# Optimization experiments

Hardware: AMD Instinct MI355X
Metric: run time of the kernel (lower is better)

Reference implementation:

```python
import jax, jax.numpy as jnp
import numpy as np

H = 256      # HIDDEN_DIM
F_IN = 16    # input_dim
B = 512
S = 168      # encoder sequence length
T = 24       # PRED_LEN


def _lstm_cell(x, h, c, w_ih, w_hh, b):
    # torch gate order: i, f, g, o
    g = x @ w_ih.T + h @ w_hh.T + b
    i, f, gg, o = jnp.split(g, 4, axis=-1)
    c_new = jax.nn.sigmoid(f) * c + jax.nn.sigmoid(i) * jnp.tanh(gg)
    h_new = jax.nn.sigmoid(o) * jnp.tanh(c_new)
    return h_new, c_new


def _lstm_layer(x, w_ih, w_hh, b):
    # x: [S, B, in] -> outputs [S, B, H], final (h, c)
    Bv, Hv = x.shape[1], w_hh.shape[1]
    init = (jnp.zeros((Bv, Hv), x.dtype), jnp.zeros((Bv, Hv), x.dtype))
    def step(carry, xt):
        h, c = _lstm_cell(xt, carry[0], carry[1], w_ih, w_hh, b)
        return (h, c), h
    (h, c), ys = jax.lax.scan(step, init, x)
    return ys, h, c


def setup_inputs() -> dict:
    key = jax.random.key(0)
    ks = jax.random.split(key, 24)
    s = 1.0 / np.sqrt(H)
    u = lambda k, shape: jax.random.uniform(k, shape, jnp.float32, -s, s)
    inp = {}
    inp['src'] = jax.random.normal(ks[0], (B, S, F_IN), jnp.float32)
    # encoder LSTM (2 layers); biases b_ih + b_hh fused into one vector
    inp['enc_w_ih0'] = u(ks[1], (4 * H, F_IN))
    inp['enc_w_hh0'] = u(ks[2], (4 * H, H))
    inp['enc_b0'] = u(ks[3], (4 * H,))
    inp['enc_w_ih1'] = u(ks[4], (4 * H, H))
    inp['enc_w_hh1'] = u(ks[5], (4 * H, H))
    inp['enc_b1'] = u(ks[6], (4 * H,))
    # decoder LSTM (2 layers), input_size = 1 + H
    inp['dec_w_ih0'] = u(ks[7], (4 * H, 1 + H))
    inp['dec_w_hh0'] = u(ks[8], (4 * H, H))
    inp['dec_b0'] = u(ks[9], (4 * H,))
    inp['dec_w_ih1'] = u(ks[10], (4 * H, H))
    inp['dec_w_hh1'] = u(ks[11], (4 * H, H))
    inp['dec_b1'] = u(ks[12], (4 * H,))
    # attention: Linear(2H -> H), v: Linear(H -> 1, no bias), position bias
    inp['attn_w'] = u(ks[13], (H, 2 * H))
    inp['attn_b'] = u(ks[14], (H,))
    inp['attn_v'] = u(ks[15], (H,))
    inp['pos_bias'] = jax.random.normal(ks[16], (H,), jnp.float32)
    # fc_out: Linear(H -> 1)
    inp['fc_w'] = u(ks[17], (1, H))
    inp['fc_b'] = u(ks[18], (1,))
    return inp


def reference(src, enc_w_ih0, enc_w_hh0, enc_b0, enc_w_ih1, enc_w_hh1, enc_b1,
              dec_w_ih0, dec_w_hh0, dec_b0, dec_w_ih1, dec_w_hh1, dec_b1,
              attn_w, attn_b, attn_v, pos_bias, fc_w, fc_b):
    x = jnp.transpose(src, (1, 0, 2))  # [S, B, F]
    y0, _, _ = _lstm_layer(x, enc_w_ih0, enc_w_hh0, enc_b0)
    enc_out_t, h1e, c1e = _lstm_layer(y0, enc_w_ih1, enc_w_hh1, enc_b1)
    # also need final state of layer 0 for decoder init
    h0e, c0e = y0[-1], None
    # recompute layer-0 final cell state: rerun scan carry output
    # (cheap alternative: _lstm_layer returns (ys, h, c); reuse it)
    _, h0e, c0e = _lstm_layer(x, enc_w_ih0, enc_w_hh0, enc_b0)
    enc_out = jnp.transpose(enc_out_t, (1, 0, 2))  # [B, S, H]

    We, Wd = attn_w[:, :H], attn_w[:, H:]
    enc_proj = jnp.einsum('bsh,gh->bsg', enc_out, We)  # precomputed encoder projection
    dec_in0 = src[:, -1, -1:]  # [B, 1]

    def dec_step(carry, t):
        h0, c0, h1, c1, dec_in = carry
        # additive attention using top-layer decoder hidden
        e = jnp.tanh(enc_proj + (h1 @ Wd.T + attn_b)[:, None, :])
        e = e + pos_bias[None, None, :] * (t / 24.0)
        w = jax.nn.softmax(e @ attn_v, axis=1)              # [B, S]
        ctx = jnp.einsum('bs,bsh->bh', w, enc_out)          # [B, H]
        x0 = jnp.concatenate([dec_in, ctx], axis=1)          # [B, 1+H]
        h0n, c0n = _lstm_cell(x0, h0, c0, dec_w_ih0, dec_w_hh0, dec_b0)
        h1n, c1n = _lstm_cell(h0n, h1, c1, dec_w_ih1, dec_w_hh1, dec_b1)
        pred = h1n @ fc_w.T + fc_b                           # [B, 1]
        # NOTE: the gated blend of decoder_output in the source is dead code
        # (the blended tensor is never used), so it is omitted here.
        return (h0n, c0n, h1n, c1n, pred), pred

    ts = jnp.arange(T, dtype=src.dtype)
    _, preds = jax.lax.scan(dec_step, (h0e, c0e, h1e, c1e, dec_in0), ts)
    return jnp.transpose(preds, (1, 0, 2))  # [B, T, 1]
```

## Files before the change

### kernel.cpp

```cpp
#include <hip/hip_runtime.h>
#include <hip/hip_fp16.h>
#include <math.h>

#define BB 512
#define HH 256
#define SS 168
#define TT 24
#define NBLK 256
#define NTHR 256
typedef unsigned long long ull;
typedef unsigned short u16;
#define BH 131072ull

#define O_Y0  0ull
#define O_H1  262144ull
#define O_H0  524288ull
#define O_CTX 786432ull
#define O_W0  933888ull
#define O_W1  1261568ull
#define O_WP  2834432ull
#define O_WDT 2835456ull
#define O_BP  2900992ull
#define O_E16 2905088ull
#define O_P16 13915136ull

typedef float f32x4 __attribute__((ext_vector_type(4)));
typedef float v2f __attribute__((ext_vector_type(2)));
typedef unsigned int ru4 __attribute__((ext_vector_type(4)));

__device__ __forceinline__ float sigf(float x) { return 1.f / (1.f + expf(-x)); }

#define AR __ATOMIC_RELAXED
#define SCA __HIP_MEMORY_SCOPE_AGENT
__device__ __forceinline__ int aLd(int* p) { return __hip_atomic_load(p, AR, SCA); }
__device__ __forceinline__ int aAdd(int* p, int v) { return __hip_atomic_fetch_add(p, v, AR, SCA); }

__device__ __forceinline__ float2 ld2(const float* p) {
  ull raw = __hip_atomic_load((const ull*)p, AR, SCA);
  float2 v; v.x = __uint_as_float((unsigned)raw); v.y = __uint_as_float((unsigned)(raw >> 32));
  return v;
}
__device__ __forceinline__ float ld1(const float* p) {
  unsigned raw = __hip_atomic_load((const unsigned*)p, AR, SCA);
  return __uint_as_float(raw);
}
__device__ __forceinline__ void st1(float* p, float v) {
  __hip_atomic_store((unsigned*)p, __float_as_uint(v), AR, SCA);
}
__device__ __forceinline__ void sth(__half* p, __half v) {
  __hip_atomic_store((unsigned short*)p, __half_as_ushort(v), AR, SCA);
}
__device__ __forceinline__ void stu(unsigned* p, unsigned v) {
  __hip_atomic_store(p, v, AR, SCA);
}

__device__ __forceinline__ void ld_h(const float* p, v2f& a, v2f& b) {
  asm volatile("global_load_dwordx2 %0, %2, off sc0 sc1\n\t"
               "global_load_dwordx2 %1, %3, off sc0 sc1"
               : "=&v"(a), "=&v"(b) : "v"(p), "v"(p + 16) : "memory");
}
struct W4 { ru4 v[4]; };
__device__ __forceinline__ void ld_w4(const u16* ph, const u16* pl, W4& w) {
  asm volatile("global_load_dwordx4 %0, %4, off\n\t"
               "global_load_dwordx4 %1, %5, off\n\t"
               "global_load_dwordx4 %2, %6, off\n\t"
               "global_load_dwordx4 %3, %7, off"
               : "=&v"(w.v[0]), "=&v"(w.v[1]), "=&v"(w.v[2]), "=&v"(w.v[3])
               : "v"(ph), "v"(ph + 8), "v"(pl), "v"(pl + 8) : "memory");
}
#define VMW(n) asm volatile("s_waitcnt vmcnt(" #n ")" ::: "memory")

#define MFMA(d, a, b) asm volatile("v_mfma_f32_16x16x32_bf16 %0, %1, %2, %0" \
                                   : "+v"(d) : "v"(a), "v"(b))
#define TOUCH(x) asm volatile("" : "+v"(x))

__device__ __forceinline__ void poll(int* f, int tgt) {
  while (aLd(f) < tgt) __builtin_amdgcn_s_sleep(1);
}
__device__ __forceinline__ void flag_arrive(int* f) {
  asm volatile("s_waitcnt vmcnt(0)" ::: "memory");
  __syncthreads();
  if (threadIdx.x == 0) aAdd(f, 1);
}
__device__ __forceinline__ void flag_wait2(int* f0, int t0, int* f1, int t1) {
  if (threadIdx.x == 0 && f0) poll(f0, t0);
  if (threadIdx.x == 64 && f1) poll(f1, t1);
  __syncthreads();
}

struct SMT {
  union {
    struct { unsigned WsH[128][20]; unsigned WsL[128][20]; float Ht[32][36]; } m;
    struct { float As[32][65];  float Bs[32][65]; } g;
    struct { float h1s[256], qs[256], vs[256], sc[192], ctxs[512], sred[4]; } at;
  };
};

__device__ __forceinline__ void fma16(float acc[4][4], const float4 hv, const float4 wv) {
  acc[0][0] += hv.x * wv.x; acc[0][1] += hv.x * wv.y; acc[0][2] += hv.x * wv.z; acc[0][3] += hv.x * wv.w;
  acc[1][0] += hv.y * wv.x; acc[1][1] += hv.y * wv.y; acc[1][2] += hv.y * wv.z; acc[1][3] += hv.y * wv.w;
  acc[2][0] += hv.z * wv.x; acc[2][1] += hv.z * wv.y; acc[2][2] += hv.z * wv.z; acc[2][3] += hv.z * wv.w;
  acc[3][0] += hv.w * wv.x; acc[3][1] += hv.w * wv.y; acc[3][2] += hv.w * wv.z; acc[3][3] += hv.w * wv.w;
}

__device__ __forceinline__ unsigned rne16(unsigned u) {
  return (u + 0x7fffu + ((u >> 16) & 1u)) >> 16;
}
__device__ __forceinline__ void split8v(const f32x4 a, const f32x4 b, ru4& hi, ru4& lo) {
#pragma unroll
  for (int j = 0; j < 4; j++) {
    const float x = (j < 2) ? a[2 * j] : b[2 * j - 4];
    const float y = (j < 2) ? a[2 * j + 1] : b[2 * j - 3];
    const unsigned hx = rne16(__float_as_uint(x)), hy = rne16(__float_as_uint(y));
    const float rx = x - __uint_as_float(hx << 16);
    const float ry = y - __uint_as_float(hy << 16);
    hi[j] = (hx & 0xffffu) | (hy << 16);
    lo[j] = (rne16(__float_as_uint(rx)) & 0xffffu) | (rne16(__float_as_uint(ry)) << 16);
  }
}

__device__ __forceinline__ void comp_mfma(SMT& sm, int wq, int w1, int l15, int l4,
                                          f32x4 acc[4])
{
  const int hr = w1 * 16 + l15;
  const f32x4 hv0 = *(const f32x4*)&sm.m.Ht[hr][l4 * 8];
  const f32x4 hv1 = *(const f32x4*)&sm.m.Ht[hr][l4 * 8 + 4];
  ru4 bhi, blo;
  split8v(hv0, hv1, bhi, blo);
  asm volatile("s_nop 1" : "+v"(bhi), "+v"(blo));
#pragma unroll
  for (int g = 0; g < 4; g++) {
    const int cr = wq * 64 + g * 16 + l15;
    ru4 ah = *(const ru4*)&sm.m.WsH[cr][l4 * 4];
    ru4 al = *(const ru4*)&sm.m.WsL[cr][l4 * 4];
    MFMA(acc[g], ah, bhi);
    MFMA(acc[g], ah, blo);
    MFMA(acc[g], al, bhi);
  }
}

#define STW(wv) do { \
  *(ru4*)&sm.m.WsH[cgt][kt * 8]     = (wv).v[0]; \
  *(ru4*)&sm.m.WsH[cgt][kt * 8 + 4] = (wv).v[1]; \
  *(ru4*)&sm.m.WsL[cgt][kt * 8]     = (wv).v[2]; \
  *(ru4*)&sm.m.WsL[cgt][kt * 8 + 4] = (wv).v[3]; } while (0)
#define STH(a, b) do { \
  sm.m.Ht[r][p2 * 2]      = (a)[0]; sm.m.Ht[r][p2 * 2 + 1]  = (a)[1]; \
  sm.m.Ht[r][p2 * 2 + 16] = (b)[0]; sm.m.Ht[r][p2 * 2 + 17] = (b)[1]; } while (0)

__device__ void gemm_pipe(const u16* wbh, const u16* wbl,
                          const float* hb0, const float* hb1,
                          int NC, int nc0, f32x4 acc[4], SMT& sm,
                          int wq, int w1, int l15, int l4)
{
  const int tid = threadIdx.x;
  const int r = tid & 31, p2 = tid >> 5;
  const int cgt = tid & 127, kt = tid >> 7;
  const float* h1p = hb1 - (ull)nc0 * 32;
#define HBk(k) (((k) < nc0) ? (hb0 + (k) * 32) : (h1p + (k) * 32))
  W4 wr0, wr1, wr2, wr3;
  v2f h0a, h0b, h1a, h1b, h2a, h2b, h3a, h3b;
  ld_w4(wbh, wbl, wr0);
  ld_h(HBk(0), h0a, h0b);
  ld_w4(wbh + 32, wbl + 32, wr1);
  ld_h(HBk(1), h1a, h1b);
  ld_h(HBk(2), h2a, h2b);
  for (int c = 0; c < NC; c += 4) {
    VMW(8);
    STW(wr0); STH(h0a, h0b);
    __syncthreads();
    ld_w4(wbh + (c + 2) * 32, wbl + (c + 2) * 32, wr2);
    ld_h(HBk(c + 3), h3a, h3b);
    comp_mfma(sm, wq, w1, l15, l4, acc);
    __syncthreads();
    VMW(8);
    STW(wr1); STH(h1a, h1b);
    __syncthreads();
    ld_w4(wbh + (c + 3) * 32, wbl + (c + 3) * 32, wr3);
    ld_h(HBk(c + 4), h0a, h0b);
    comp_mfma(sm, wq, w1, l15, l4, acc);
    __syncthreads();
    VMW(8);
    STW(wr2); STH(h2a, h2b);
    __syncthreads();
    ld_w4(wbh + (c + 4) * 32, wbl + (c + 4) * 32, wr0);
    ld_h(HBk(c + 5), h1a, h1b);
    comp_mfma(sm, wq, w1, l15, l4, acc);
    __syncthreads();
    VMW(8);
    STW(wr3); STH(h3a, h3b);
    __syncthreads();
    ld_w4(wbh + (c + 5) * 32, wbl + (c + 5) * 32, wr1);
    ld_h(HBk(c + 6), h2a, h2b);
    comp_mfma(sm, wq, w1, l15, l4, acc);
    __syncthreads();
  }
  asm volatile("s_waitcnt vmcnt(0)" ::: "memory");
  asm volatile("s_nop 7\n\ts_nop 7"
               : "+v"(acc[0]), "+v"(acc[1]), "+v"(acc[2]), "+v"(acc[3]));
#undef HBk
}

__device__ __forceinline__ void lstm_epi4(f32x4 acc[4], float cR[4], int row, int ubase, int l4,
                                          float* hout, __half* e16, int sstep)
{
#pragma unroll
  for (int g = 0; g < 4; g++) {
    const int u = ubase + g * 4 + l4;
    const float iv = sigf(acc[g][0]), fv = sigf(acc[g][1]);
    const float gv = tanhf(acc[g][2]), ov = sigf(acc[g][3]);
    const float cn = fv * cR[g] + iv * gv;
    cR[g] = cn;
    const float hn = ov * tanhf(cn);
    st1(hout + (ull)row * 256 + u, hn);
    if (e16) sth(e16 + ((ull)row * SS + sstep) * 256 + u, __float2half(hn));
  }
}

__device__ void attn_fc(int row, int t, int slot, const float* h1r, const float* wdT,
                        const float* attn_b, const float* attn_v,
                        const __half* P16, const __half* E16,
                        const float* fc_w, const float* fc_b,
                        float* ctxb, float* out, SMT& sm)
{
  const int tid = threadIdx.x;
  __syncthreads();
  if (tid < 128) {
    float2 v = ld2(h1r + (ull)slot * BH + (ull)row * 256 + tid * 2);
    sm.at.h1s[tid * 2] = v.x; sm.at.h1s[tid * 2 + 1] = v.y;
  }
  __syncthreads();
  if (t >= 1 && tid < 64) {
    float a = 0.f;
#pragma unroll
    for (int j = 0; j < 4; j++) a += sm.at.h1s[tid + 64 * j] * fc_w[tid + 64 * j];
#pragma unroll
    for (int m = 32; m >= 1; m >>= 1) a += __shfl_xor(a, m, 64);
    if (tid == 0) {
      const float p = a + fc_b[0];
      out[(ull)row * TT + (t - 1)] = p;
      st1(ctxb + (ull)row * 288 + 256, p);
    }
  }
  if (t >= TT) return;
  float qv = attn_b[tid];
  for (int k = 0; k < 256; k += 4) {
    qv += sm.at.h1s[k]     * wdT[(ull)(k)     * 256 + tid];
    qv += sm.at.h1s[k + 1] * wdT[(ull)(k + 1) * 256 + tid];
    qv += sm.at.h1s[k + 2] * wdT[(ull)(k + 2) * 256 + tid];
    qv += sm.at.h1s[k + 3] * wdT[(ull)(k + 3) * 256 + tid];
  }
  sm.at.qs[tid] = qv;
  sm.at.vs[tid] = attn_v[tid];
  __syncthreads();
  const int wv = tid >> 6, lane = tid & 63;
  for (int s = wv; s < SS; s += 4) {
    const __half2* Pr = (const __half2*)(P16 + ((ull)row * SS + s) * 256);
    float a = 0.f;
#pragma unroll
    for (int jj = 0; jj < 2; jj++) {
      const int i2 = lane + 64 * jj;
      const float2 pv = __half22float2(Pr[i2]);
      const int g0 = i2 * 2;
      a += sm.at.vs[g0] * tanhf(pv.x + sm.at.qs[g0]);
      a += sm.at.vs[g0 + 1] * tanhf(pv.y + sm.at.qs[g0 + 1]);
    }
#pragma unroll
    for (int m = 32; m >= 1; m >>= 1) a += __shfl_xor(a, m, 64);
    if (lane == 0) sm.at.sc[s] = a;
  }
  __syncthreads();
  if (tid < 64) {
    float m = -1e30f;
    for (int i = tid; i < SS; i += 64) m = fmaxf(m, sm.at.sc[i]);
#pragma unroll
    for (int mm = 32; mm >= 1; mm >>= 1) m = fmaxf(m, __shfl_xor(m, mm, 64));
    if (tid == 0) sm.at.sred[0] = m;
  }
  __syncthreads();
  const float smax = sm.at.sred[0];
  if (tid < SS) sm.at.sc[tid] = expf(sm.at.sc[tid] - smax);
  __syncthreads();
  if (tid < 64) {
    float ssum = 0.f;
    for (int i = tid; i < SS; i += 64) ssum += sm.at.sc[i];
#pragma unroll
    for (int mm = 32; mm >= 1; mm >>= 1) ssum += __shfl_xor(ssum, mm, 64);
    if (tid == 0) sm.at.sred[1] = ssum;
  }
  __syncthreads();
  const float rinv = 1.f / sm.at.sred[1];
  const int u2 = tid & 127, sh = tid >> 7;
  float cx = 0.f, cy = 0.f;
  for (int s = sh * 84; s < sh * 84 + 84; s++) {
    const float w = sm.at.sc[s] * rinv;
    const float2 ev = __half22float2(*(const __half2*)(E16 + ((ull)row * SS + s) * 256 + u2 * 2));
    cx += w * ev.x; cy += w * ev.y;
  }
  sm.at.ctxs[sh * 256 + u2 * 2] = cx;
  sm.at.ctxs[sh * 256 + u2 * 2 + 1] = cy;
  __syncthreads();
  st1(ctxb + (ull)row * 288 + tid, sm.at.ctxs[tid] + sm.at.ctxs[256 + tid]);
}

__device__ void proj_tile(const __half* E16, const float* attn_w, __half* P16,
                          int m0, int n0, SMT& sm)
{
  const int tid = threadIdx.x;
  const int mq = tid & 15, nq = tid >> 4;
  const int li = tid & 63, kq = tid >> 6;
  float acc[4][4] = {{0.f}};
  for (int k0 = 0; k0 < 256; k0 += 32) {
    float4 raw = *(const float4*)(E16 + (ull)(m0 + li) * 256 + k0 + kq * 8);
    const __half* hp = (const __half*)&raw;
#pragma unroll
    for (int i = 0; i < 8; i++) sm.g.As[kq * 8 + i][li] = __half2float(hp[i]);
    const float* gb = attn_w + (ull)(n0 + li) * 512 + k0 + kq * 8;
    const float4 v0 = *(const float4*)gb, v1 = *(const float4*)(gb + 4);
    sm.g.Bs[kq * 8 + 0][li] = v0.x; sm.g.Bs[kq * 8 + 1][li] = v0.y;
    sm.g.Bs[kq * 8 + 2][li] = v0.z; sm.g.Bs[kq * 8 + 3][li] = v0.w;
    sm.g.Bs[kq * 8 + 4][li] = v1.x; sm.g.Bs[kq * 8 + 5][li] = v1.y;
    sm.g.Bs[kq * 8 + 6][li] = v1.z; sm.g.Bs[kq * 8 + 7][li] = v1.w;
    __syncthreads();
#pragma unroll 8
    for (int kk = 0; kk < 32; kk++) {
      const float4 a4 = *(const float4*)&sm.g.As[kk][mq * 4];
      const float4 b4 = *(const float4*)&sm.g.Bs[kk][nq * 4];
      fma16(acc, a4, b4);
    }
    __syncthreads();
  }
#pragma unroll
  for (int i = 0; i < 4; i++) {
    const int m = m0 + mq * 4 + i;
#pragma unroll
    for (int j = 0; j < 2; j++) {
      __half2 h2; h2.x = __float2half(acc[i][j * 2]); h2.y = __float2half(acc[i][j * 2 + 1]);
      stu((unsigned*)(P16 + (ull)m * 256 + n0 + nq * 4) + j, *(unsigned*)&h2);
    }
  }
}

__global__ __launch_bounds__(256, 1) void seq2seq_pipe(
    const float* __restrict__ src,
    const float* __restrict__ attn_w, const float* __restrict__ attn_b,
    const float* __restrict__ attn_v,
    const float* __restrict__ fc_w, const float* __restrict__ fc_b,
    float* __restrict__ out, int* __restrict__ ib)
{
  __shared__ SMT sm;
  const int blk = blockIdx.x;
  const int tid = threadIdx.x;
  float* fb = (float*)ib + 65536;
  float* y0r  = fb + O_Y0;
  float* h1r  = fb + O_H1;
  float* h0r  = fb + O_H0;
  float* zb   = h0r + BH;
  float* ctxb = fb + O_CTX;
  const u16* whi0 = (const u16*)(fb + O_W0);
  const u16* wlo0 = whi0 + 1024ull * 320;
  const u16* whi1 = (const u16*)(fb + O_W1);
  const u16* wlo1 = whi1 + 1024ull * 512;
  const u16* dhi0 = whi1 + 2ull * 1024 * 512;
  const u16* dlo0 = whi1 + 3ull * 1024 * 512;
  const u16* dhi1 = whi1 + 4ull * 1024 * 512;
  const u16* dlo1 = whi1 + 5ull * 1024 * 512;
  const float* wp  = fb + O_WP;
  const float* wdT = fb + O_WDT;
  const float* bp  = fb + O_BP;
  __half* E16 = (__half*)(fb + O_E16);
  __half* P16 = (__half*)(fb + O_P16);
  const int g = blk >> 5, m = blk & 31;
  const int rowg = g * 64;
  int* gf = ib + g * 1024;
  int* ife = gf;
  int* ifa = gf + 704; int* ifh0 = gf + 736; int* ifh1 = gf + 768; int* ifp = gf + 900;

  const int lm = (m < 16) ? m : (m - 16);
  const int row0 = rowg + (lm & 1) * 32;
  const int gc0 = (lm >> 1) * 128;
  const int w = tid >> 6;
  const int l15 = tid & 15, l4 = (tid >> 4) & 3;
  const int wq = w >> 1, w1 = w & 1;
  const int gcw = gc0 + wq * 64;
  const int myrow = row0 + w1 * 16 + l15;
  const int ubase = gcw >> 2;
  const int r = tid & 31;
  const int cgt = tid & 127, kt = tid >> 7;

  float cReg[4] = {0.f, 0.f, 0.f, 0.f};

  for (int t = 0; t <= SS; t++) {
    flag_wait2(t ? ife + (t - 1) : nullptr, 32, nullptr, 0);
    if (m < 16) {
      if (t < SS) {
        f32x4 acc[4];
#pragma unroll
        for (int gg = 0; gg < 4; gg++) {
          acc[gg] = *(const f32x4*)(bp + gcw + gg * 16 + l4 * 4);
          TOUCH(acc[gg]);
        }
        {
          W4 wx;
          ld_w4(whi0 + (ull)(gc0 + cgt) * 320 + kt * 16,
                wlo0 + (ull)(gc0 + cgt) * 320 + kt * 16, wx);
          VMW(0);
          *(ru4*)&sm.m.WsH[cgt][kt * 8]     = wx.v[0];
          *(ru4*)&sm.m.WsH[cgt][kt * 8 + 4] = wx.v[1];
          *(ru4*)&sm.m.WsL[cgt][kt * 8]     = wx.v[2];
          *(ru4*)&sm.m.WsL[cgt][kt * 8 + 4] = wx.v[3];
          const int f = tid >> 5;
          sm.m.Ht[r][f]      = src[((ull)(row0 + r) * SS + t) * 16 + f];
          sm.m.Ht[r][f + 8]  = src[((ull)(row0 + r) * SS + t) * 16 + f + 8];
          sm.m.Ht[r][f + 16] = 0.f;
          sm.m.Ht[r][f + 24] = 0.f;
          __syncthreads();
          comp_mfma(sm, wq, w1, l15, l4, acc);
          __syncthreads();
        }
        const float* ysrc = (t == 0) ? zb : (y0r + (ull)((t + 1) & 1) * BH);
        const float* hb0 = ysrc + (ull)(row0 + r) * 256 + (tid >> 5) * 2;
        gemm_pipe(whi0 + (ull)(gc0 + cgt) * 320 + 32 + kt * 16,
                  wlo0 + (ull)(gc0 + cgt) * 320 + 32 + kt * 16,
                  hb0, hb0, 8, 8, acc, sm, wq, w1, l15, l4);
        lstm_epi4(acc, cReg, myrow, ubase, l4, y0r + (ull)(t & 1) * BH, nullptr, 0);
      }
    } else {
      if (t >= 1) {
        const int s = t - 1;
        f32x4 acc[4];
#pragma unroll
        for (int gg = 0; gg < 4; gg++) {
          acc[gg] = *(const f32x4*)(bp + 1024 + gcw + gg * 16 + l4 * 4);
          TOUCH(acc[gg]);
        }
        const float* ysrc = y0r + (ull)(s & 1) * BH;
        const float* hsrc = (s == 0) ? zb : (h1r + (ull)((s + 1) & 1) * BH);
        const float* hb0 = ysrc + (ull)(row0 + r) * 256 + (tid >> 5) * 2;
        const float* hb1 = hsrc + (ull)(row0 + r) * 256 + (tid >> 5) * 2;
        gemm_pipe(whi1 + (ull)(gc0 + cgt) * 512 + kt * 16,
                  wlo1 + (ull)(gc0 + cgt) * 512 + kt * 16,
                  hb0, hb1, 16, 8, acc, sm, wq, w1, l15, l4);
        lstm_epi4(acc, cReg, myrow, ubase, l4, h1r + (ull)(s & 1) * BH, E16, s);
      }
    }
    flag_arrive(ife + t);
  }

  if (tid == 0) poll(ife + SS, 32);
  __syncthreads();
  {
    const int em0 = rowg * SS;
    for (int tau = m; tau < 672; tau += 32)
      proj_tile(E16, attn_w, P16, em0 + (tau >> 2) * 64, (tau & 3) * 64, sm);
  }
  flag_arrive(ifp);

  for (int t = 0; t <= TT; t++) {
    if (t == 0) flag_wait2(ifp, 32, nullptr, 0);
    else flag_wait2(ifh1 + (t - 1), 16, nullptr, 0);
    const int slot = (t + 1) & 1;
    attn_fc(rowg + 2 * m,     t, slot, h1r, wdT, attn_b, attn_v, P16, E16, fc_w, fc_b, ctxb, out, sm);
    attn_fc(rowg + 2 * m + 1, t, slot, h1r, wdT, attn_b, attn_v, P16, E16, fc_w, fc_b, ctxb, out, sm);
    if (t == TT) break;
    flag_arrive(ifa + t);
    if (m < 16) {
      flag_wait2(ifa + t, 32, t ? ifh0 + (t - 1) : nullptr, 16);
      f32x4 acc[4];
#pragma unroll
      for (int gg = 0; gg < 4; gg++) {
        acc[gg] = *(const f32x4*)(bp + 2048 + gcw + gg * 16 + l4 * 4);
        TOUCH(acc[gg]);
      }
      const float* h0src = (t == 0) ? (y0r + BH) : (h0r + (ull)((t + 1) & 1) * BH);
      const float* hb0 = ctxb + (ull)(row0 + r) * 288 + (tid >> 5) * 2;
      const float* hb1 = h0src + (ull)(row0 + r) * 256 + (tid >> 5) * 2;
      gemm_pipe(dhi0 + (ull)(gc0 + cgt) * 512 + kt * 16,
                dlo0 + (ull)(gc0 + cgt) * 512 + kt * 16,
                hb0, hb1, 16, 8, acc, sm, wq, w1, l15, l4);
      const float p = ld1(ctxb + (ull)myrow * 288 + 256);
#pragma unroll
      for (int gg = 0; gg < 4; gg++) {
        const f32x4 wpv = *(const f32x4*)(wp + gcw + gg * 16 + l4 * 4);
        acc[gg] = acc[gg] + wpv * p;
      }
      lstm_epi4(acc, cReg, myrow, ubase, l4, h0r + (ull)(t & 1) * BH, nullptr, 0);
      flag_arrive(ifh0 + t);
    } else {
      flag_wait2(ifh0 + t, 16, t ? ifh1 + (t - 1) : nullptr, 16);
      f32x4 acc[4];
#pragma unroll
      for (int gg = 0; gg < 4; gg++) {
        acc[gg] = *(const f32x4*)(bp + 3072 + gcw + gg * 16 + l4 * 4);
        TOUCH(acc[gg]);
      }
      const float* hb0 = h0r + (ull)(t & 1) * BH + (ull)(row0 + r) * 256 + (tid >> 5) * 2;
      const float* hb1 = h1r + (ull)((t + 1) & 1) * BH + (ull)(row0 + r) * 256 + (tid >> 5) * 2;
      gemm_pipe(dhi1 + (ull)(gc0 + cgt) * 512 + kt * 16,
                dlo1 + (ull)(gc0 + cgt) * 512 + kt * 16,
                hb0, hb1, 16, 8, acc, sm, wq, w1, l15, l4);
      lstm_epi4(acc, cReg, myrow, ubase, l4, h1r + (ull)(t & 1) * BH, nullptr, 0);
      flag_arrive(ifh1 + t);
    }
  }
}

__device__ __forceinline__ void split_store(float v, u16* hi, u16* lo, ull i) {
  const unsigned u = __float_as_uint(v);
  const unsigned hb = (u + 0x7fffu + ((u >> 16) & 1u)) >> 16;
  const float rr = v - __uint_as_float(hb << 16);
  const unsigned ur = __float_as_uint(rr);
  const unsigned lb = (ur + 0x7fffu + ((ur >> 16) & 1u)) >> 16;
  hi[i] = (u16)hb; lo[i] = (u16)lb;
}

__global__ void init_all(
    const float* __restrict__ src,
    const float* __restrict__ ewih0, const float* __restrict__ ewhh0, const float* __restrict__ eb0,
    const float* __restrict__ ewih1, const float* __restrict__ ewhh1, const float* __restrict__ eb1,
    const float* __restrict__ dwih0, const float* __restrict__ dwhh0, const float* __restrict__ db0,
    const float* __restrict__ dwih1, const float* __restrict__ dwhh1, const float* __restrict__ db1,
    const float* __restrict__ attn_w, int* __restrict__ ib)
{
  const int gid = blockIdx.x * 256 + threadIdx.x;
  const int NG = 1024 * 256;
  float* fb = (float*)ib + 65536;
  u16* whi0 = (u16*)(fb + O_W0);
  u16* wlo0 = whi0 + 1024ull * 320;
  u16* whi1 = (u16*)(fb + O_W1);
  u16* wlo1 = whi1 + 1024ull * 512;
  u16* dhi0 = whi1 + 2ull * 1024 * 512;
  u16* dlo0 = whi1 + 3ull * 1024 * 512;
  u16* dhi1 = whi1 + 4ull * 1024 * 512;
  u16* dlo1 = whi1 + 5ull * 1024 * 512;
  float* wpd = fb + O_WP;

  for (int i = gid; i < 8192; i += NG) ib[i] = 0;
  for (int i = gid; i < (int)BH; i += NG) fb[O_H0 + BH + i] = 0.f;
  for (int i = gid; i < 1024 * 320; i += NG) {
    const int cg = i / 320, k = i - cg * 320, j = (cg & 3) * 256 + (cg >> 2);
    float v = 0.f;
    if (k < 16) v = ewih0[(ull)j * 16 + k];
    else if (k >= 32 && k < 288) v = ewhh0[(ull)j * 256 + (k - 32)];
    split_store(v, whi0, wlo0, i);
  }
  for (int i = gid; i < 1024 * 512; i += NG) {
    const int cg = i >> 9, k = i & 511, j = (cg & 3) * 256 + (cg >> 2);
    split_store((k < 256) ? ewih1[(ull)j * 256 + k] : ewhh1[(ull)j * 256 + k - 256], whi1, wlo1, i);
    split_store((k < 256) ? dwih0[(ull)j * 257 + 1 + k] : dwhh0[(ull)j * 256 + k - 256], dhi0, dlo0, i);
    split_store((k < 256) ? dwih1[(ull)j * 256 + k] : dwhh1[(ull)j * 256 + k - 256], dhi1, dlo1, i);
  }
  for (int i = gid; i < 1024; i += NG) {
    const int j = (i & 3) * 256 + (i >> 2);
    wpd[i] = dwih0[(ull)j * 257];
  }
  for (int i = gid; i < 256 * 256; i += NG) {
    const int k = i >> 8, gg = i & 255;
    fb[O_WDT + i] = attn_w[(ull)gg * 512 + 256 + k];
  }
  for (int i = gid; i < 4096; i += NG) {
    const int set = i >> 10, cg = i & 1023, j = (cg & 3) * 256 + (cg >> 2);
    const float* bsrc = (set == 0) ? eb0 : (set == 1) ? eb1 : (set == 2) ? db0 : db1;
    fb[O_BP + i] = bsrc[j];
  }
  for (int i = gid; i < 512; i += NG)
    fb[O_CTX + (ull)i * 288 + 256] = src[((ull)i * SS + 167) * 16 + 15];
}

extern "C" void kernel_launch(void* const* d_in, const int* in_sizes, int n_in,
                              void* d_out, int out_size, void* d_ws, size_t ws_size,
                              hipStream_t stream)
{
  const float* src    = (const float*)d_in[0];
  const float* ewih0  = (const float*)d_in[1];
  const float* ewhh0  = (const float*)d_in[2];
  const float* eb0    = (const float*)d_in[3];
  const float* ewih1  = (const float*)d_in[4];
  const float* ewhh1  = (const float*)d_in[5];
  const float* eb1    = (const float*)d_in[6];
  const float* dwih0  = (const float*)d_in[7];
  const float* dwhh0  = (const float*)d_in[8];
  const float* db0    = (const float*)d_in[9];
  const float* dwih1  = (const float*)d_in[10];
  const float* dwhh1  = (const float*)d_in[11];
  const float* db1    = (const float*)d_in[12];
  const float* attn_w = (const float*)d_in[13];
  const float* attn_b = (const float*)d_in[14];
  const float* attn_v = (const float*)d_in[15];
  const float* fc_w   = (const float*)d_in[17];
  const float* fc_b   = (const float*)d_in[18];
  float* out = (float*)d_out;
  int* ib    = (int*)d_ws;

  init_all<<<1024, 256, 0, stream>>>(src, ewih0, ewhh0, eb0, ewih1, ewhh1, eb1,
                                     dwih0, dwhh0, db0, dwih1, dwhh1, db1, attn_w, ib);

  void* args[] = {
    (void*)&src, (void*)&attn_w, (void*)&attn_b, (void*)&attn_v,
    (void*)&fc_w, (void*)&fc_b, (void*)&out, (void*)&ib,
  };
  hipError_t lerr = hipLaunchCooperativeKernel((const void*)seq2seq_pipe, dim3(NBLK), dim3(NTHR),
                                               args, 0, stream);
  if (lerr != hipSuccess) {
    hipLaunchKernelGGL(seq2seq_pipe, dim3(NBLK), dim3(NTHR), 0, stream,
                       src, attn_w, attn_b, attn_v, fc_w, fc_b, out, ib);
  }
}
```

Before: 7.867 ms.

## Double threads per block to 512 and split per-thread GEMM and attention work

Raises the persistent kernel's block size from 256 to 512 threads. Each warp now covers 32 gate columns instead of 64 in the MFMA LSTM GEMM, and per-thread weight and hidden loads are halved. The attention score and context loops are spread over 8 waves, with four partial context sums reduced at the end. The intent is more latency hiding and shorter per-thread serial chains in the latency-bound recurrent steps, at the cost of more registers per block, idle threads in the projection tile, and heavier barriers.

```diff
diff --git a/kernel.cpp b/kernel.cpp
--- a/kernel.cpp
+++ b/kernel.cpp
@@ -7,7 +7,7 @@
 #define SS 168
 #define TT 24
 #define NBLK 256
-#define NTHR 256
+#define NTHR 512
 typedef unsigned long long ull;
 typedef unsigned short u16;
 #define BH 131072ull
@@ -54,19 +54,14 @@
   __hip_atomic_store(p, v, AR, SCA);
 }
 
-__device__ __forceinline__ void ld_h(const float* p, v2f& a, v2f& b) {
-  asm volatile("global_load_dwordx2 %0, %2, off sc0 sc1\n\t"
-               "global_load_dwordx2 %1, %3, off sc0 sc1"
-               : "=&v"(a), "=&v"(b) : "v"(p), "v"(p + 16) : "memory");
-}
-struct W4 { ru4 v[4]; };
-__device__ __forceinline__ void ld_w4(const u16* ph, const u16* pl, W4& w) {
-  asm volatile("global_load_dwordx4 %0, %4, off\n\t"
-               "global_load_dwordx4 %1, %5, off\n\t"
-               "global_load_dwordx4 %2, %6, off\n\t"
-               "global_load_dwordx4 %3, %7, off"
-               : "=&v"(w.v[0]), "=&v"(w.v[1]), "=&v"(w.v[2]), "=&v"(w.v[3])
-               : "v"(ph), "v"(ph + 8), "v"(pl), "v"(pl + 8) : "memory");
+__device__ __forceinline__ void ld_h2(const float* p, v2f& a) {
+  asm volatile("global_load_dwordx2 %0, %1, off sc0 sc1"
+               : "=&v"(a) : "v"(p) : "memory");
+}
+__device__ __forceinline__ void ld_w2(const u16* ph, const u16* pl, ru4& h, ru4& l) {
+  asm volatile("global_load_dwordx4 %0, %2, off\n\t"
+               "global_load_dwordx4 %1, %3, off"
+               : "=&v"(h), "=&v"(l) : "v"(ph), "v"(pl) : "memory");
 }
 #define VMW(n) asm volatile("s_waitcnt vmcnt(" #n ")" ::: "memory")
 
@@ -92,7 +87,7 @@
   union {
     struct { unsigned WsH[128][20]; unsigned WsL[128][20]; float Ht[32][36]; } m;
     struct { float As[32][65];  float Bs[32][65]; } g;
-    struct { float h1s[256], qs[256], vs[256], sc[192], ctxs[512], sred[4]; } at;
+    struct { float h1s[256], qs[256], vs[256], sc[192], ctxs[1024], sred[4]; } at;
   };
 };
 
@@ -120,7 +115,7 @@
 }
 
 __device__ __forceinline__ void comp_mfma(SMT& sm, int wq, int w1, int l15, int l4,
-                                          f32x4 acc[4])
+                                          f32x4 acc[2])
 {
   const int hr = w1 * 16 + l15;
   const f32x4 hv0 = *(const f32x4*)&sm.m.Ht[hr][l4 * 8];
@@ -129,8 +124,8 @@
   split8v(hv0, hv1, bhi, blo);
   asm volatile("s_nop 1" : "+v"(bhi), "+v"(blo));
 #pragma unroll
-  for (int g = 0; g < 4; g++) {
-    const int cr = wq * 64 + g * 16 + l15;
+  for (int g = 0; g < 2; g++) {
+    const int cr = wq * 32 + g * 16 + l15;
     ru4 ah = *(const ru4*)&sm.m.WsH[cr][l4 * 4];
     ru4 al = *(const ru4*)&sm.m.WsL[cr][l4 * 4];
     MFMA(acc[g], ah, bhi);
@@ -139,18 +134,15 @@
   }
 }
 
-#define STW(wv) do { \
-  *(ru4*)&sm.m.WsH[cgt][kt * 8]     = (wv).v[0]; \
-  *(ru4*)&sm.m.WsH[cgt][kt * 8 + 4] = (wv).v[1]; \
-  *(ru4*)&sm.m.WsL[cgt][kt * 8]     = (wv).v[2]; \
-  *(ru4*)&sm.m.WsL[cgt][kt * 8 + 4] = (wv).v[3]; } while (0)
-#define STH(a, b) do { \
-  sm.m.Ht[r][p2 * 2]      = (a)[0]; sm.m.Ht[r][p2 * 2 + 1]  = (a)[1]; \
-  sm.m.Ht[r][p2 * 2 + 16] = (b)[0]; sm.m.Ht[r][p2 * 2 + 17] = (b)[1]; } while (0)
+#define STW(wh, wl) do { \
+  *(ru4*)&sm.m.WsH[cgt][kt * 4] = (wh); \
+  *(ru4*)&sm.m.WsL[cgt][kt * 4] = (wl); } while (0)
+#define STH(a) do { \
+  sm.m.Ht[r][p2 * 2] = (a)[0]; sm.m.Ht[r][p2 * 2 + 1] = (a)[1]; } while (0)
 
 __device__ void gemm_pipe(const u16* wbh, const u16* wbl,
                           const float* hb0, const float* hb1,
-                          int NC, int nc0, f32x4 acc[4], SMT& sm,
+                          int NC, int nc0, f32x4 acc[2], SMT& sm,
                           int wq, int w1, int l15, int l4)
 {
   const int tid = threadIdx.x;
@@ -158,54 +150,53 @@
   const int cgt = tid & 127, kt = tid >> 7;
   const float* h1p = hb1 - (ull)nc0 * 32;
 #define HBk(k) (((k) < nc0) ? (hb0 + (k) * 32) : (h1p + (k) * 32))
-  W4 wr0, wr1, wr2, wr3;
-  v2f h0a, h0b, h1a, h1b, h2a, h2b, h3a, h3b;
-  ld_w4(wbh, wbl, wr0);
-  ld_h(HBk(0), h0a, h0b);
-  ld_w4(wbh + 32, wbl + 32, wr1);
-  ld_h(HBk(1), h1a, h1b);
-  ld_h(HBk(2), h2a, h2b);
+  ru4 wh0, wl0, wh1, wl1, wh2, wl2, wh3, wl3;
+  v2f h0, h1, h2, h3;
+  ld_w2(wbh,      wbl,      wh0, wl0);
+  ld_h2(HBk(0), h0);
+  ld_w2(wbh + 32, wbl + 32, wh1, wl1);
+  ld_h2(HBk(1), h1);
+  ld_h2(HBk(2), h2);
   for (int c = 0; c < NC; c += 4) {
-    VMW(8);
-    STW(wr0); STH(h0a, h0b);
-    __syncthreads();
-    ld_w4(wbh + (c + 2) * 32, wbl + (c + 2) * 32, wr2);
-    ld_h(HBk(c + 3), h3a, h3b);
+    VMW(4);
+    STW(wh0, wl0); STH(h0);
+    __syncthreads();
+    ld_w2(wbh + (c + 2) * 32, wbl + (c + 2) * 32, wh2, wl2);
+    ld_h2(HBk(c + 3), h3);
     comp_mfma(sm, wq, w1, l15, l4, acc);
     __syncthreads();
-    VMW(8);
-    STW(wr1); STH(h1a, h1b);
-    __syncthreads();
-    ld_w4(wbh + (c + 3) * 32, wbl + (c + 3) * 32, wr3);
-    ld_h(HBk(c + 4), h0a, h0b);
+    VMW(4);
+    STW(wh1, wl1); STH(h1);
+    __syncthreads();
+    ld_w2(wbh + (c + 3) * 32, wbl + (c + 3) * 32, wh3, wl3);
+    ld_h2(HBk(c + 4), h0);
     comp_mfma(sm, wq, w1, l15, l4, acc);
     __syncthreads();
-    VMW(8);
-    STW(wr2); STH(h2a, h2b);
-    __syncthreads();
-    ld_w4(wbh + (c + 4) * 32, wbl + (c + 4) * 32, wr0);
-    ld_h(HBk(c + 5), h1a, h1b);
+    VMW(4);
+    STW(wh2, wl2); STH(h2);
+    __syncthreads();
+    ld_w2(wbh + (c + 4) * 32, wbl + (c + 4) * 32, wh0, wl0);
+    ld_h2(HBk(c + 5), h1);
     comp_mfma(sm, wq, w1, l15, l4, acc);
     __syncthreads();
-    VMW(8);
-    STW(wr3); STH(h3a, h3b);
-    __syncthreads();
-    ld_w4(wbh + (c + 5) * 32, wbl + (c + 5) * 32, wr1);
-    ld_h(HBk(c + 6), h2a, h2b);
+    VMW(4);
+    STW(wh3, wl3); STH(h3);
+    __syncthreads();
+    ld_w2(wbh + (c + 5) * 32, wbl + (c + 5) * 32, wh1, wl1);
+    ld_h2(HBk(c + 6), h2);
     comp_mfma(sm, wq, w1, l15, l4, acc);
     __syncthreads();
   }
   asm volatile("s_waitcnt vmcnt(0)" ::: "memory");
-  asm volatile("s_nop 7\n\ts_nop 7"
-               : "+v"(acc[0]), "+v"(acc[1]), "+v"(acc[2]), "+v"(acc[3]));
+  asm volatile("s_nop 7\n\ts_nop 7" : "+v"(acc[0]), "+v"(acc[1]));
 #undef HBk
 }
 
-__device__ __forceinline__ void lstm_epi4(f32x4 acc[4], float cR[4], int row, int ubase, int l4,
+__device__ __forceinline__ void lstm_epi2(f32x4 acc[2], float cR[2], int row, int ubase, int l4,
                                           float* hout, __half* e16, int sstep)
 {
 #pragma unroll
-  for (int g = 0; g < 4; g++) {
+  for (int g = 0; g < 2; g++) {
     const int u = ubase + g * 4 + l4;
     const float iv = sigf(acc[g][0]), fv = sigf(acc[g][1]);
     const float gv = tanhf(acc[g][2]), ov = sigf(acc[g][3]);
@@ -243,18 +234,20 @@
     }
   }
   if (t >= TT) return;
-  float qv = attn_b[tid];
-  for (int k = 0; k < 256; k += 4) {
-    qv += sm.at.h1s[k]     * wdT[(ull)(k)     * 256 + tid];
-    qv += sm.at.h1s[k + 1] * wdT[(ull)(k + 1) * 256 + tid];
-    qv += sm.at.h1s[k + 2] * wdT[(ull)(k + 2) * 256 + tid];
-    qv += sm.at.h1s[k + 3] * wdT[(ull)(k + 3) * 256 + tid];
-  }
-  sm.at.qs[tid] = qv;
-  sm.at.vs[tid] = attn_v[tid];
+  if (tid < 256) {
+    float qv = attn_b[tid];
+    for (int k = 0; k < 256; k += 4) {
+      qv += sm.at.h1s[k]     * wdT[(ull)(k)     * 256 + tid];
+      qv += sm.at.h1s[k + 1] * wdT[(ull)(k + 1) * 256 + tid];
+      qv += sm.at.h1s[k + 2] * wdT[(ull)(k + 2) * 256 + tid];
+      qv += sm.at.h1s[k + 3] * wdT[(ull)(k + 3) * 256 + tid];
+    }
+    sm.at.qs[tid] = qv;
+    sm.at.vs[tid] = attn_v[tid];
+  }
   __syncthreads();
   const int wv = tid >> 6, lane = tid & 63;
-  for (int s = wv; s < SS; s += 4) {
+  for (int s = wv; s < SS; s += 8) {
     const __half2* Pr = (const __half2*)(P16 + ((ull)row * SS + s) * 256);
     float a = 0.f;
 #pragma unroll
@@ -292,7 +285,7 @@
   const float rinv = 1.f / sm.at.sred[1];
   const int u2 = tid & 127, sh = tid >> 7;
   float cx = 0.f, cy = 0.f;
-  for (int s = sh * 84; s < sh * 84 + 84; s++) {
+  for (int s = sh * 42; s < sh * 42 + 42; s++) {
     const float w = sm.at.sc[s] * rinv;
     const float2 ev = __half22float2(*(const __half2*)(E16 + ((ull)row * SS + s) * 256 + u2 * 2));
     cx += w * ev.x; cy += w * ev.y;
@@ -300,48 +293,57 @@
   sm.at.ctxs[sh * 256 + u2 * 2] = cx;
   sm.at.ctxs[sh * 256 + u2 * 2 + 1] = cy;
   __syncthreads();
-  st1(ctxb + (ull)row * 288 + tid, sm.at.ctxs[tid] + sm.at.ctxs[256 + tid]);
+  if (tid < 256)
+    st1(ctxb + (ull)row * 288 + tid,
+        sm.at.ctxs[tid] + sm.at.ctxs[256 + tid] + sm.at.ctxs[512 + tid] + sm.at.ctxs[768 + tid]);
 }
 
 __device__ void proj_tile(const __half* E16, const float* attn_w, __half* P16,
                           int m0, int n0, SMT& sm)
 {
   const int tid = threadIdx.x;
-  const int mq = tid & 15, nq = tid >> 4;
-  const int li = tid & 63, kq = tid >> 6;
+  const bool act = tid < 256;
+  const int mq = tid & 15, nq = (tid >> 4) & 15;
+  const int li = tid & 63, kq = (tid >> 6) & 3;
   float acc[4][4] = {{0.f}};
   for (int k0 = 0; k0 < 256; k0 += 32) {
-    float4 raw = *(const float4*)(E16 + (ull)(m0 + li) * 256 + k0 + kq * 8);
-    const __half* hp = (const __half*)&raw;
-#pragma unroll
-    for (int i = 0; i < 8; i++) sm.g.As[kq * 8 + i][li] = __half2float(hp[i]);
-    const float* gb = attn_w + (ull)(n0 + li) * 512 + k0 + kq * 8;
-    const float4 v0 = *(const float4*)gb, v1 = *(const float4*)(gb + 4);
-    sm.g.Bs[kq * 8 + 0][li] = v0.x; sm.g.Bs[kq * 8 + 1][li] = v0.y;
-    sm.g.Bs[kq * 8 + 2][li] = v0.z; sm.g.Bs[kq * 8 + 3][li] = v0.w;
-    sm.g.Bs[kq * 8 + 4][li] = v1.x; sm.g.Bs[kq * 8 + 5][li] = v1.y;
-    sm.g.Bs[kq * 8 + 6][li] = v1.z; sm.g.Bs[kq * 8 + 7][li] = v1.w;
-    __syncthreads();
+    if (act) {
+      float4 raw = *(const float4*)(E16 + (ull)(m0 + li) * 256 + k0 + kq * 8);
+      const __half* hp = (const __half*)&raw;
+#pragma unroll
+      for (int i = 0; i < 8; i++) sm.g.As[kq * 8 + i][li] = __half2float(hp[i]);
+      const float* gb = attn_w + (ull)(n0 + li) * 512 + k0 + kq * 8;
+      const float4 v0 = *(const float4*)gb, v1 = *(const float4*)(gb + 4);
+      sm.g.Bs[kq * 8 + 0][li] = v0.x; sm.g.Bs[kq * 8 + 1][li] = v0.y;
+      sm.g.Bs[kq * 8 + 2][li] = v0.z; sm.g.Bs[kq * 8 + 3][li] = v0.w;
+      sm.g.Bs[kq * 8 + 4][li] = v1.x; sm.g.Bs[kq * 8 + 5][li] = v1.y;
+      sm.g.Bs[kq * 8 + 6][li] = v1.z; sm.g.Bs[kq * 8 + 7][li] = v1.w;
+    }
+    __syncthreads();
+    if (act) {
 #pragma unroll 8
-    for (int kk = 0; kk < 32; kk++) {
-      const float4 a4 = *(const float4*)&sm.g.As[kk][mq * 4];
-      const float4 b4 = *(const float4*)&sm.g.Bs[kk][nq * 4];
-      fma16(acc, a4, b4);
-    }
-    __syncthreads();
-  }
-#pragma unroll
-  for (int i = 0; i < 4; i++) {
-    const int m = m0 + mq * 4 + i;
-#pragma unroll
-    for (int j = 0; j < 2; j++) {
-      __half2 h2; h2.x = __float2half(acc[i][j * 2]); h2.y = __float2half(acc[i][j * 2 + 1]);
-      stu((unsigned*)(P16 + (ull)m * 256 + n0 + nq * 4) + j, *(unsigned*)&h2);
-    }
-  }
-}
-
-__global__ __launch_bounds__(256, 1) void seq2seq_pipe(
+      for (int kk = 0; kk < 32; kk++) {
+        const float4 a4 = *(const float4*)&sm.g.As[kk][mq * 4];
+        const float4 b4 = *(const float4*)&sm.g.Bs[kk][nq * 4];
+        fma16(acc, a4, b4);
+      }
+    }
+    __syncthreads();
+  }
+  if (act) {
+#pragma unroll
+    for (int i = 0; i < 4; i++) {
+      const int m = m0 + mq * 4 + i;
+#pragma unroll
+      for (int j = 0; j < 2; j++) {
+        __half2 h2; h2.x = __float2half(acc[i][j * 2]); h2.y = __float2half(acc[i][j * 2 + 1]);
+        stu((unsigned*)(P16 + (ull)m * 256 + n0 + nq * 4) + j, *(unsigned*)&h2);
+      }
+    }
+  }
+}
+
+__global__ __launch_bounds__(512, 1) void seq2seq_pipe(
     const float* __restrict__ src,
     const float* __restrict__ attn_w, const float* __restrict__ attn_b,
     const float* __restrict__ attn_v,
@@ -381,56 +383,52 @@
   const int gc0 = (lm >> 1) * 128;
   const int w = tid >> 6;
   const int l15 = tid & 15, l4 = (tid >> 4) & 3;
-  const int wq = w >> 1, w1 = w & 1;
-  const int gcw = gc0 + wq * 64;
+  const int w1 = w & 1, wq = w >> 1;
+  const int gcw = gc0 + wq * 32;
   const int myrow = row0 + w1 * 16 + l15;
   const int ubase = gcw >> 2;
   const int r = tid & 31;
   const int cgt = tid & 127, kt = tid >> 7;
 
-  float cReg[4] = {0.f, 0.f, 0.f, 0.f};
+  float cReg[2] = {0.f, 0.f};
 
   for (int t = 0; t <= SS; t++) {
     flag_wait2(t ? ife + (t - 1) : nullptr, 32, nullptr, 0);
     if (m < 16) {
       if (t < SS) {
-        f32x4 acc[4];
-#pragma unroll
-        for (int gg = 0; gg < 4; gg++) {
+        f32x4 acc[2];
+#pragma unroll
+        for (int gg = 0; gg < 2; gg++) {
           acc[gg] = *(const f32x4*)(bp + gcw + gg * 16 + l4 * 4);
           TOUCH(acc[gg]);
         }
         {
-          W4 wx;
-          ld_w4(whi0 + (ull)(gc0 + cgt) * 320 + kt * 16,
-                wlo0 + (ull)(gc0 + cgt) * 320 + kt * 16, wx);
+          ru4 wxh, wxl;
+          ld_w2(whi0 + (ull)(gc0 + cgt) * 320 + kt * 8,
+                wlo0 + (ull)(gc0 + cgt) * 320 + kt * 8, wxh, wxl);
           VMW(0);
-          *(ru4*)&sm.m.WsH[cgt][kt * 8]     = wx.v[0];
-          *(ru4*)&sm.m.WsH[cgt][kt * 8 + 4] = wx.v[1];
-          *(ru4*)&sm.m.WsL[cgt][kt * 8]     = wx.v[2];
-          *(ru4*)&sm.m.WsL[cgt][kt * 8 + 4] = wx.v[3];
+          *(ru4*)&sm.m.WsH[cgt][kt * 4] = wxh;
+          *(ru4*)&sm.m.WsL[cgt][kt * 4] = wxl;
           const int f = tid >> 5;
           sm.m.Ht[r][f]      = src[((ull)(row0 + r) * SS + t) * 16 + f];
-          sm.m.Ht[r][f + 8]  = src[((ull)(row0 + r) * SS + t) * 16 + f + 8];
           sm.m.Ht[r][f + 16] = 0.f;
-          sm.m.Ht[r][f + 24] = 0.f;
           __syncthreads();
           comp_mfma(sm, wq, w1, l15, l4, acc);
           __syncthreads();
         }
         const float* ysrc = (t == 0) ? zb : (y0r + (ull)((t + 1) & 1) * BH);
         const float* hb0 = ysrc + (ull)(row0 + r) * 256 + (tid >> 5) * 2;
-        gemm_pipe(whi0 + (ull)(gc0 + cgt) * 320 + 32 + kt * 16,
-                  wlo0 + (ull)(gc0 + cgt) * 320 + 32 + kt * 16,
+        gemm_pipe(whi0 + (ull)(gc0 + cgt) * 320 + 32 + kt * 8,
+                  wlo0 + (ull)(gc0 + cgt) * 320 + 32 + kt * 8,
                   hb0, hb0, 8, 8, acc, sm, wq, w1, l15, l4);
-        lstm_epi4(acc, cReg, myrow, ubase, l4, y0r + (ull)(t & 1) * BH, nullptr, 0);
+        lstm_epi2(acc, cReg, myrow, ubase, l4, y0r + (ull)(t & 1) * BH, nullptr, 0);
       }
     } else {
       if (t >= 1) {
         const int s = t - 1;
-        f32x4 acc[4];
-#pragma unroll
-        for (int gg = 0; gg < 4; gg++) {
+        f32x4 acc[2];
+#pragma unroll
+        for (int gg = 0; gg < 2; gg++) {
           acc[gg] = *(const f32x4*)(bp + 1024 + gcw + gg * 16 + l4 * 4);
           TOUCH(acc[gg]);
         }
@@ -438,10 +436,10 @@
         const float* hsrc = (s == 0) ? zb : (h1r + (ull)((s + 1) & 1) * BH);
         const float* hb0 = ysrc + (ull)(row0 + r) * 256 + (tid >> 5) * 2;
         const float* hb1 = hsrc + (ull)(row0 + r) * 256 + (tid >> 5) * 2;
-        gemm_pipe(whi1 + (ull)(gc0 + cgt) * 512 + kt * 16,
-                  wlo1 + (ull)(gc0 + cgt) * 512 + kt * 16,
+        gemm_pipe(whi1 + (ull)(gc0 + cgt) * 512 + kt * 8,
+                  wlo1 + (ull)(gc0 + cgt) * 512 + kt * 8,
                   hb0, hb1, 16, 8, acc, sm, wq, w1, l15, l4);
-        lstm_epi4(acc, cReg, myrow, ubase, l4, h1r + (ull)(s & 1) * BH, E16, s);
+        lstm_epi2(acc, cReg, myrow, ubase, l4, h1r + (ull)(s & 1) * BH, E16, s);
       }
     }
     flag_arrive(ife + t);
@@ -466,40 +464,40 @@
     flag_arrive(ifa + t);
     if (m < 16) {
       flag_wait2(ifa + t, 32, t ? ifh0 + (t - 1) : nullptr, 16);
-      f32x4 acc[4];
-#pragma unroll
-      for (int gg = 0; gg < 4; gg++) {
+      f32x4 acc[2];
+#pragma unroll
+      for (int gg = 0; gg < 2; gg++) {
         acc[gg] = *(const f32x4*)(bp + 2048 + gcw + gg * 16 + l4 * 4);
         TOUCH(acc[gg]);
       }
       const float* h0src = (t == 0) ? (y0r + BH) : (h0r + (ull)((t + 1) & 1) * BH);
       const float* hb0 = ctxb + (ull)(row0 + r) * 288 + (tid >> 5) * 2;
       const float* hb1 = h0src + (ull)(row0 + r) * 256 + (tid >> 5) * 2;
-      gemm_pipe(dhi0 + (ull)(gc0 + cgt) * 512 + kt * 16,
-                dlo0 + (ull)(gc0 + cgt) * 512 + kt * 16,
+      gemm_pipe(dhi0 + (ull)(gc0 + cgt) * 512 + kt * 8,
+                dlo0 + (ull)(gc0 + cgt) * 512 + kt * 8,
                 hb0, hb1, 16, 8, acc, sm, wq, w1, l15, l4);
       const float p = ld1(ctxb + (ull)myrow * 288 + 256);
 #pragma unroll
-      for (int gg = 0; gg < 4; gg++) {
+      for (int gg = 0; gg < 2; gg++) {
         const f32x4 wpv = *(const f32x4*)(wp + gcw + gg * 16 + l4 * 4);
         acc[gg] = acc[gg] + wpv * p;
       }
-      lstm_epi4(acc, cReg, myrow, ubase, l4, h0r + (ull)(t & 1) * BH, nullptr, 0);
+      lstm_epi2(acc, cReg, myrow, ubase, l4, h0r + (ull)(t & 1) * BH, nullptr, 0);
       flag_arrive(ifh0 + t);
     } else {
       flag_wait2(ifh0 + t, 16, t ? ifh1 + (t - 1) : nullptr, 16);
-      f32x4 acc[4];
-#pragma unroll
-      for (int gg = 0; gg < 4; gg++) {
+      f32x4 acc[2];
+#pragma unroll
+      for (int gg = 0; gg < 2; gg++) {
         acc[gg] = *(const f32x4*)(bp + 3072 + gcw + gg * 16 + l4 * 4);
         TOUCH(acc[gg]);
       }
       const float* hb0 = h0r + (ull)(t & 1) * BH + (ull)(row0 + r) * 256 + (tid >> 5) * 2;
       const float* hb1 = h1r + (ull)((t + 1) & 1) * BH + (ull)(row0 + r) * 256 + (tid >> 5) * 2;
-      gemm_pipe(dhi1 + (ull)(gc0 + cgt) * 512 + kt * 16,
-                dlo1 + (ull)(gc0 + cgt) * 512 + kt * 16,
+      gemm_pipe(dhi1 + (ull)(gc0 + cgt) * 512 + kt * 8,
+                dlo1 + (ull)(gc0 + cgt) * 512 + kt * 8,
                 hb0, hb1, 16, 8, acc, sm, wq, w1, l15, l4);
-      lstm_epi4(acc, cReg, myrow, ubase, l4, h1r + (ull)(t & 1) * BH, nullptr, 0);
+      lstm_epi2(acc, cReg, myrow, ubase, l4, h1r + (ull)(t & 1) * BH, nullptr, 0);
       flag_arrive(ifh1 + t);
     }
   }
```

After: 7.029 ms. 1.12x faster.
